# Kernel tuning notes

Hardware: AMD Instinct MI355X
Metric: run time of the kernel (lower is better)

Reference implementation:

```python
import jax, jax.numpy as jnp
import numpy as np

N_NODES = 50000
N_EDGES = 1_600_000
IN_DIM = 256
HIDDEN = 256
OUT_DIM = 48
K = 10
ALPHA = 0.5


def _ppr_temp(K, alpha):
    # PPR init from GPR_prop: temp[k] = alpha*(1-alpha)^k, temp[K] = (1-alpha)^K
    t = alpha * (1 - alpha) ** np.arange(K + 1, dtype=np.float32)
    t[-1] = (1 - alpha) ** K
    return jnp.asarray(t, dtype=jnp.float32)


def setup_inputs() -> dict:
    key = jax.random.key(0)
    ks = jax.random.split(key, 7)
    x = jax.random.normal(ks[0], (N_NODES, IN_DIM), dtype=jnp.float32)
    edge_index = jax.random.randint(ks[1], (2, N_EDGES), 0, N_NODES, dtype=jnp.int64)
    # Linear layers (torch Linear: y = x @ W.T + b); store as [in, out]
    lim1 = 1.0 / np.sqrt(IN_DIM)
    W1 = jax.random.uniform(ks[2], (IN_DIM, HIDDEN), jnp.float32, -lim1, lim1)
    b1 = jax.random.uniform(ks[3], (HIDDEN,), jnp.float32, -lim1, lim1)
    lim2 = 1.0 / np.sqrt(HIDDEN)
    W2 = jax.random.uniform(ks[4], (HIDDEN, OUT_DIM), jnp.float32, -lim2, lim2)
    b2 = jax.random.uniform(ks[5], (OUT_DIM,), jnp.float32, -lim2, lim2)
    temp = _ppr_temp(K, ALPHA)
    return {"x": x, "edge_index": edge_index, "W1": W1, "b1": b1,
            "W2": W2, "b2": b2, "temp": temp}


def reference(x, edge_index, W1, b1, W2, b2, temp):
    N = x.shape[0]
    # MLP head (dropout in eval mode -> identity)
    h = jax.nn.relu(x @ W1 + b1)
    h = h @ W2 + b2  # [N, OUT_DIM]

    # GCN normalization with self-loops: norm_e = deg^-1/2[src] * deg^-1/2[dst]
    loops = jnp.arange(N, dtype=edge_index.dtype)
    src = jnp.concatenate([edge_index[0], loops])
    dst = jnp.concatenate([edge_index[1], loops])
    deg = jnp.zeros((N,), dtype=h.dtype).at[dst].add(1.0)
    dinv = jax.lax.rsqrt(jnp.maximum(deg, 1e-12))
    norm = (dinv[src] * dinv[dst])[:, None]  # [E+N, 1]

    # K-hop propagation with learned gamma mixing
    def step(carry, gamma):
        hk, hidden = carry
        msg = norm * hk[src]                              # gather + scale
        hk = jax.ops.segment_sum(msg, dst, num_segments=N)  # scatter-add
        return (hk, hidden + gamma * hk), None

    (_, hidden), _ = jax.lax.scan(step, (h, temp[0] * h), temp[1:])
    return jax.nn.log_softmax(hidden, axis=1)
```

## Files before the change

### kernel.cpp

```cpp
#include <hip/hip_runtime.h>
#include <hip/hip_fp16.h>
#include <math.h>

#define BSH    9
#define BNODES 512
#define NBMAX  128
#define CAP2   24576
#define ECHUNK 6144

typedef short bf16x8 __attribute__((ext_vector_type(8)));
typedef float f32x4 __attribute__((ext_vector_type(4)));

__device__ __forceinline__ unsigned f2b(float f) {
    union { float f; unsigned u; } x; x.f = f;
    return (x.u + 0x7fffu + ((x.u >> 16) & 1u)) >> 16;
}


__global__ __launch_bounds__(256) void k_zero(int* __restrict__ p, int n) {
    int i = blockIdx.x * 256 + threadIdx.x;
    if (i < n) p[i] = 0;
}


__global__ __launch_bounds__(256) void k_castx(const float4* __restrict__ x, uint4* __restrict__ xb, int n8) {
    int i = blockIdx.x * 256 + threadIdx.x;
    if (i >= n8) return;
    float4 f0 = x[2 * i], f1 = x[2 * i + 1];
    uint4 o;
    o.x = f2b(f0.x) | (f2b(f0.y) << 16);
    o.y = f2b(f0.z) | (f2b(f0.w) << 16);
    o.z = f2b(f1.x) | (f2b(f1.y) << 16);
    o.w = f2b(f1.z) | (f2b(f1.w) << 16);
    xb[i] = o;
}

__global__ __launch_bounds__(256) void k_castw(const float* __restrict__ W1, const float* __restrict__ W2,
                                               unsigned short* __restrict__ w1t, unsigned short* __restrict__ w2t) {
    int i = blockIdx.x * 256 + threadIdx.x;
    if (i < 65536) {
        int n = i >> 8, k = i & 255;
        w1t[i] = (unsigned short)f2b(W1[k * 256 + n]);
    } else if (i < 65536 + 12288) {
        int j = i - 65536;
        int n = j >> 8, k = j & 255;
        w2t[j] = (unsigned short)f2b(W2[k * 48 + n]);
    }
}


__global__ __launch_bounds__(256) void k_bin(const int* __restrict__ src, const int* __restrict__ dst,
                                             int* __restrict__ bktcnt, unsigned* __restrict__ stage,
                                             int E, int NB) {
    __shared__ unsigned ecache[ECHUNK];
    __shared__ int lcnt[NBMAX], lbase[NBMAX], lcur[NBMAX];
    const int t = threadIdx.x;
    for (int i = t; i < NBMAX; i += 256) { lcnt[i] = 0; lcur[i] = 0; }
    const int e0 = blockIdx.x * ECHUNK;
    const int m = min(ECHUNK, E - e0);
    __syncthreads();
    for (int i = t; i < m; i += 256) {
        int s = src[e0 + i], d = dst[e0 + i];
        ecache[i] = ((unsigned)d << 16) | (unsigned)s;
        atomicAdd(&lcnt[d >> BSH], 1);
    }
    __syncthreads();
    if (t < NB) lbase[t] = lcnt[t] ? atomicAdd(&bktcnt[t], lcnt[t]) : 0;
    __syncthreads();
    for (int i = t; i < m; i += 256) {
        unsigned p = ecache[i];
        int b = (int)(p >> (16 + BSH));
        int pos = lbase[b] + atomicAdd(&lcur[b], 1);
        if (pos < CAP2) stage[(size_t)b * CAP2 + pos] = p;
    }
}


__global__ __launch_bounds__(512) void k_cnt(const unsigned* __restrict__ stage,
                                             const int* __restrict__ bktcnt,
                                             int* __restrict__ cnt,
                                             float* __restrict__ dinv, float* __restrict__ dinv2,
                                             float* __restrict__ sdeg, int N) {
    __shared__ int dcnt[BNODES];
    const int b = blockIdx.x, t = threadIdx.x;
    dcnt[t] = 0;
    __syncthreads();
    const int m = min(bktcnt[b], CAP2);
    const unsigned* st = stage + (size_t)b * CAP2;
    for (int i = t; i < m; i += 512)
        atomicAdd(&dcnt[(st[i] >> 16) & (BNODES - 1)], 1);
    __syncthreads();
    int node = b * BNODES + t;
    if (node <= N) {
        int c = dcnt[t];
        cnt[node] = c;
        float d = (float)c + 1.0f;
        float r = rsqrtf(d);
        dinv[node] = r;
        dinv2[node] = r * r;
        sdeg[node] = d * r;
    }
}


__global__ __launch_bounds__(256) void k_scan1(const int* __restrict__ cnt, int* __restrict__ rowptr,
                                               int* __restrict__ blk, int NT) {
    __shared__ int s[256];
    int t = threadIdx.x, i = blockIdx.x * 256 + t;
    int v = (i < NT) ? ((cnt[i] + 7) & ~7) : 0;
    s[t] = v; __syncthreads();
#pragma unroll
    for (int off = 1; off < 256; off <<= 1) {
        int x = (t >= off) ? s[t - off] : 0; __syncthreads();
        s[t] += x; __syncthreads();
    }
    if (i < NT) rowptr[i] = s[t] - v;
    if (t == 255) blk[blockIdx.x] = s[255];
}

__global__ __launch_bounds__(256) void k_scan2(int* __restrict__ blk, int nb) {
    __shared__ int s[256];
    int t = threadIdx.x;
    int v = (t < nb) ? blk[t] : 0;
    s[t] = v; __syncthreads();
#pragma unroll
    for (int off = 1; off < 256; off <<= 1) {
        int x = (t >= off) ? s[t - off] : 0; __syncthreads();
        s[t] += x; __syncthreads();
    }
    if (t < nb) blk[t] = s[t] - v;
}

__global__ __launch_bounds__(256) void k_scan3(int* __restrict__ rowptr, const int* __restrict__ blk, int NT) {
    int i = blockIdx.x * 256 + threadIdx.x;
    if (i < NT) rowptr[i] += blk[blockIdx.x];
}


__global__ __launch_bounds__(512) void k_place(const unsigned* __restrict__ stage,
                                               const int* __restrict__ bktcnt,
                                               const int* __restrict__ rowptr,
                                               unsigned short* __restrict__ csr, int N) {
    __shared__ int lcur[BNODES];
    const int b = blockIdx.x, t = threadIdx.x;
    const int node = b * BNODES + t;
    lcur[t] = (node < N) ? rowptr[node] : 0;
    __syncthreads();
    const int m = min(bktcnt[b], CAP2);
    const unsigned* st = stage + (size_t)b * CAP2;
    for (int i = t; i < m; i += 512) {
        unsigned p = st[i];
        int dl = (int)((p >> 16) & (BNODES - 1));
        int pos = atomicAdd(&lcur[dl], 1);
        csr[pos] = (unsigned short)(p & 0xffffu);
    }
    __syncthreads();
    if (node < N) {
        int e1 = rowptr[node + 1];
        for (int i = lcur[t]; i < e1; ++i) csr[i] = (unsigned short)N;
    }
}


__global__ __launch_bounds__(256) void k_mgemm1(const unsigned short* __restrict__ xb,
                                                const unsigned short* __restrict__ w1t,
                                                const float* __restrict__ bias,
                                                unsigned short* __restrict__ h1b, int M) {
    __shared__ unsigned short sbuf[128 * 136];
    unsigned short* As = sbuf;
    unsigned short* Bs = sbuf + 128 * 40;
    const int t = threadIdx.x;
    const int bm = blockIdx.x * 128;
    const int bn = blockIdx.y * 128;
    const int w = t >> 6, lane = t & 63;
    const int q = lane >> 4, l16 = lane & 15;

    f32x4 acc[2][8] = {};
    const int ar0 = t >> 2;
    const int kc  = t & 3;
    const int swz_st = ((kc ^ (ar0 & 3)) * 8);
    int gr0 = bm + ar0;       if (gr0 >= M) gr0 = M - 1;
    int gr1 = bm + ar0 + 64;  if (gr1 >= M) gr1 = M - 1;
    const int swz_rd = (q ^ (l16 & 3)) * 8;

    for (int k0 = 0; k0 < 256; k0 += 32) {
        uint4 a0 = *(const uint4*)&xb[(size_t)gr0 * 256 + k0 + kc * 8];
        uint4 a1 = *(const uint4*)&xb[(size_t)gr1 * 256 + k0 + kc * 8];
        uint4 b0 = *(const uint4*)&w1t[(size_t)(bn + ar0) * 256 + k0 + kc * 8];
        uint4 b1 = *(const uint4*)&w1t[(size_t)(bn + ar0 + 64) * 256 + k0 + kc * 8];
        __syncthreads();
        *(uint4*)&As[ar0 * 40 + swz_st] = a0;
        *(uint4*)&As[(ar0 + 64) * 40 + swz_st] = a1;
        *(uint4*)&Bs[ar0 * 40 + swz_st] = b0;
        *(uint4*)&Bs[(ar0 + 64) * 40 + swz_st] = b1;
        __syncthreads();
        bf16x8 af0 = *(bf16x8*)&As[(w * 32 + l16) * 40 + swz_rd];
        bf16x8 af1 = *(bf16x8*)&As[(w * 32 + 16 + l16) * 40 + swz_rd];
#pragma unroll
        for (int j = 0; j < 8; ++j) {
            bf16x8 bf = *(bf16x8*)&Bs[(j * 16 + l16) * 40 + swz_rd];
            acc[0][j] = __builtin_amdgcn_mfma_f32_16x16x32_bf16(af0, bf, acc[0][j], 0, 0, 0);
            acc[1][j] = __builtin_amdgcn_mfma_f32_16x16x32_bf16(af1, bf, acc[1][j], 0, 0, 0);
        }
    }
    __syncthreads();
#pragma unroll
    for (int j = 0; j < 8; ++j) {
        int col = j * 16 + l16;
        float bb = bias[bn + col];
#pragma unroll
        for (int i = 0; i < 2; ++i) {
#pragma unroll
            for (int r = 0; r < 4; ++r) {
                float v = fmaxf(acc[i][j][r] + bb, 0.f);
                sbuf[(w * 32 + i * 16 + q * 4 + r) * 136 + col] = (unsigned short)f2b(v);
            }
        }
    }
    __syncthreads();
    const int row = t >> 1;
    const int ch = (t & 1) * 64;
    if (bm + row < M) {
#pragma unroll
        for (int i = 0; i < 8; ++i) {
            uint4 v = *(uint4*)&sbuf[row * 136 + ch + i * 8];
            *(uint4*)&h1b[(size_t)(bm + row) * 256 + bn + ch + i * 8] = v;
        }
    }
}


__global__ __launch_bounds__(256) void k_mgemm2(const unsigned short* __restrict__ h1b,
                                                const unsigned short* __restrict__ w2t,
                                                const float* __restrict__ bias,
                                                const float* __restrict__ dinv,
                                                __half* __restrict__ u0, int M) {
    __shared__ unsigned short As[128 * 40];
    __shared__ unsigned short Bs[48 * 40];
    const int t = threadIdx.x;
    const int bm = blockIdx.x * 128;
    const int w = t >> 6, lane = t & 63;
    const int q = lane >> 4, l16 = lane & 15;

    f32x4 acc[2][3] = {};
    const int ar0 = t >> 2;
    const int kc  = t & 3;
    const int swz_st = ((kc ^ (ar0 & 3)) * 8);
    int gr0 = bm + ar0;      if (gr0 >= M) gr0 = M - 1;
    int gr1 = bm + ar0 + 64; if (gr1 >= M) gr1 = M - 1;
    const int swz_rd = (q ^ (l16 & 3)) * 8;

    for (int k0 = 0; k0 < 256; k0 += 32) {
        uint4 a0 = *(const uint4*)&h1b[(size_t)gr0 * 256 + k0 + kc * 8];
        uint4 a1 = *(const uint4*)&h1b[(size_t)gr1 * 256 + k0 + kc * 8];
        uint4 bv;
        if (t < 192) bv = *(const uint4*)&w2t[(size_t)ar0 * 256 + k0 + kc * 8];
        __syncthreads();
        *(uint4*)&As[ar0 * 40 + swz_st] = a0;
        *(uint4*)&As[(ar0 + 64) * 40 + swz_st] = a1;
        if (t < 192) *(uint4*)&Bs[ar0 * 40 + swz_st] = bv;
        __syncthreads();
        bf16x8 af0 = *(bf16x8*)&As[(w * 32 + l16) * 40 + swz_rd];
        bf16x8 af1 = *(bf16x8*)&As[(w * 32 + 16 + l16) * 40 + swz_rd];
#pragma unroll
        for (int j = 0; j < 3; ++j) {
            bf16x8 bf = *(bf16x8*)&Bs[(j * 16 + l16) * 40 + swz_rd];
            acc[0][j] = __builtin_amdgcn_mfma_f32_16x16x32_bf16(af0, bf, acc[0][j], 0, 0, 0);
            acc[1][j] = __builtin_amdgcn_mfma_f32_16x16x32_bf16(af1, bf, acc[1][j], 0, 0, 0);
        }
    }
#pragma unroll
    for (int j = 0; j < 3; ++j) {
        int col = j * 16 + l16;
        float bb = bias[col];
#pragma unroll
        for (int i = 0; i < 2; ++i) {
#pragma unroll
            for (int r = 0; r < 4; ++r) {
                int row = bm + w * 32 + i * 16 + q * 4 + r;
                if (row < M) {
                    float v = (acc[i][j][r] + bb) * dinv[row];
                    u0[(size_t)row * 64 + col] = __float2half(v);
                }
            }
        }
    }
}


__global__ __launch_bounds__(256) void k_hop(const __half* __restrict__ u, __half* __restrict__ unxt,
                                             const int* __restrict__ rowptr,
                                             const unsigned short* __restrict__ csr,
                                             const float* __restrict__ dinv2, int NT, int N) {
    int n = blockIdx.x * 4 + (threadIdx.x >> 6);
    if (n >= NT) return;
    const int lane = threadIdx.x & 63;
    const int c = lane & 7;
    const int j = lane >> 3;

    float acc[8] = {0.f, 0.f, 0.f, 0.f, 0.f, 0.f, 0.f, 0.f};
    const int e0 = rowptr[n], e1 = rowptr[n + 1];
    for (int e = e0; e < e1; e += 48) {
        const int rem = e1 - e;
        int t0 = (int)csr[e + j];
        int t1 = (int)csr[e + 8 + j];
        int t2 = (int)csr[e + 16 + j];
        int t3 = (int)csr[e + 24 + j];
        int t4 = (int)csr[e + 32 + j];
        int t5 = (int)csr[e + 40 + j];
        int s0 = t0;
        int s1 = (rem > 8)  ? t1 : N;
        int s2 = (rem > 16) ? t2 : N;
        int s3 = (rem > 24) ? t3 : N;
        int s4 = (rem > 32) ? t4 : N;
        int s5 = (rem > 40) ? t5 : N;
        union { uint4 u4; __half2 h2[4]; } g0, g1, g2, g3, g4, g5;
        g0.u4 = *(const uint4*)(u + (size_t)s0 * 64 + c * 8);
        g1.u4 = *(const uint4*)(u + (size_t)s1 * 64 + c * 8);
        g2.u4 = *(const uint4*)(u + (size_t)s2 * 64 + c * 8);
        g3.u4 = *(const uint4*)(u + (size_t)s3 * 64 + c * 8);
        g4.u4 = *(const uint4*)(u + (size_t)s4 * 64 + c * 8);
        g5.u4 = *(const uint4*)(u + (size_t)s5 * 64 + c * 8);
#pragma unroll
        for (int i = 0; i < 4; ++i) {
            float2 f0 = __half22float2(g0.h2[i]);
            float2 f1 = __half22float2(g1.h2[i]);
            float2 f2 = __half22float2(g2.h2[i]);
            float2 f3 = __half22float2(g3.h2[i]);
            float2 f4 = __half22float2(g4.h2[i]);
            float2 f5 = __half22float2(g5.h2[i]);
            acc[2 * i]     += ((f0.x + f1.x) + (f2.x + f3.x)) + (f4.x + f5.x);
            acc[2 * i + 1] += ((f0.y + f1.y) + (f2.y + f3.y)) + (f4.y + f5.y);
        }
    }
#pragma unroll
    for (int off = 8; off < 64; off <<= 1) {
#pragma unroll
        for (int i = 0; i < 8; ++i) acc[i] += __shfl_xor(acc[i], off);
    }
    if (j == 0 && c < 6) {
        union { uint4 u4; __half2 h2[4]; } sv, ov;
        sv.u4 = *(const uint4*)(u + (size_t)n * 64 + c * 8);
        float w2 = dinv2[n];
#pragma unroll
        for (int i = 0; i < 4; ++i) {
            float2 sf = __half22float2(sv.h2[i]);
            float2 r;
            r.x = (acc[2 * i]     + sf.x) * w2;
            r.y = (acc[2 * i + 1] + sf.y) * w2;
            ov.h2[i] = __float22half2_rn(r);
        }
        *(uint4*)(unxt + (size_t)n * 64 + c * 8) = ov.u4;
    }
}


__global__ __launch_bounds__(256) void k_final(const __half* __restrict__ u0, const __half* __restrict__ u1,
                                               size_t S, const float* __restrict__ sdeg,
                                               const float* __restrict__ temp,
                                               float* __restrict__ out, int N) {
    int w = (blockIdx.x * 256 + threadIdx.x) >> 6;
    int lane = threadIdx.x & 63;
    if (w >= N) return;
    size_t base = (size_t)w * 64 + lane;
    float val = 0.f, m = -INFINITY;
    if (lane < 48) {
        float acc = temp[0] * __half2float(u0[base]);
        const __half* uk = u1;
#pragma unroll
        for (int k = 1; k <= 10; ++k) {
            acc += temp[k] * __half2float(uk[base]);
            uk += S;
        }
        val = acc * sdeg[w];
        m = val;
    }
#pragma unroll
    for (int off = 32; off; off >>= 1) m = fmaxf(m, __shfl_xor(m, off));
    float ex = (lane < 48) ? __expf(val - m) : 0.f;
    float s = ex;
#pragma unroll
    for (int off = 32; off; off >>= 1) s += __shfl_xor(s, off);
    if (lane < 48) out[(size_t)w * 48 + lane] = val - m - __logf(s);
}


extern "C" void kernel_launch(void* const* d_in, const int* in_sizes, int n_in,
                              void* d_out, int out_size, void* d_ws, size_t ws_size,
                              hipStream_t stream) {
    const float* x    = (const float*)d_in[0];
    const int*   ei   = (const int*)d_in[1];
    const float* W1   = (const float*)d_in[2];
    const float* b1   = (const float*)d_in[3];
    const float* W2   = (const float*)d_in[4];
    const float* b2   = (const float*)d_in[5];
    const float* temp = (const float*)d_in[6];
    float* out = (float*)d_out;

    const int N = in_sizes[0] / 256;
    const int E = in_sizes[1] / 2;
    const int* src = ei;
    const int* dst = ei + E;

    const int NT  = N + 1;
    const int NT2 = N + 2;
    const int NB  = (NT + BNODES - 1) >> BSH;

    char* w8 = (char*)d_ws;
    size_t NP = (size_t)((NT2 + 63) & ~63);
    int*   cnt     = (int*)w8;
    int*   bktcnt  = cnt + NP;
    int*   rowptr  = bktcnt + 128;
    int*   blk     = rowptr + NP;
    float* dinv    = (float*)(blk + 256);
    float* dinv2   = dinv + NP;
    float* sdeg    = dinv2 + NP;
    unsigned short* csr = (unsigned short*)(sdeg + NP);
    size_t csr_i   = (((size_t)E + 32 * NT) / 2 + 32 + 63) & ~(size_t)63;
    unsigned short* w1t = (unsigned short*)((int*)(sdeg + NP) + csr_i);
    unsigned short* w2t = w1t + 65536;
    unsigned short* xb  = w2t + 12288 + 64;
    size_t S       = ((size_t)NT * 64 + 127) & ~(size_t)127;
    __half* u0     = (__half*)(xb + (size_t)N * 256);
    unsigned short* h1b = (unsigned short*)(u0 + S);
    unsigned* stage = (unsigned*)h1b;
    __half* u1     = (__half*)(h1b + (size_t)N * 256);

    const int nbS = (NT2 + 255) / 256;

    k_zero  <<<(int)((NP + 128 + 255) / 256), 256, 0, stream>>>(cnt, (int)(NP + 128));
    k_bin   <<<(E + ECHUNK - 1) / ECHUNK, 256, 0, stream>>>(src, dst, bktcnt, stage, E, NB);
    k_cnt   <<<NB, 512, 0, stream>>>(stage, bktcnt, cnt, dinv, dinv2, sdeg, N);
    k_scan1 <<<nbS, 256, 0, stream>>>(cnt, rowptr, blk, NT2);
    k_scan2 <<<1, 256, 0, stream>>>(blk, nbS);
    k_scan3 <<<nbS, 256, 0, stream>>>(rowptr, blk, NT2);
    k_place <<<NB, 512, 0, stream>>>(stage, bktcnt, rowptr, csr, N);

    k_castx <<<(N * 256 / 8 + 255) / 256, 256, 0, stream>>>((const float4*)x, (uint4*)xb, N * 256 / 8);
    k_castw <<<(65536 + 12288 + 255) / 256, 256, 0, stream>>>(W1, W2, w1t, w2t);

    dim3 g1((N + 127) / 128, 2);
    k_mgemm1<<<g1, 256, 0, stream>>>(xb, w1t, b1, h1b, N);
    k_mgemm2<<<(N + 127) / 128, 256, 0, stream>>>(h1b, w2t, b2, dinv, u0, N);
    k_zero  <<<1, 64, 0, stream>>>((int*)(u0 + (size_t)N * 64), 24);

    const int hopBlocks = (NT + 3) / 4;
    for (int k = 0; k < 10; ++k) {
        const __half* cur = (k == 0) ? u0 : (u1 + (size_t)(k - 1) * S);
        __half* nxt = u1 + (size_t)k * S;
        k_hop<<<hopBlocks, 256, 0, stream>>>(cur, nxt, rowptr, csr, dinv2, NT, N);
    }

    k_final<<<(N + 3) / 4, 256, 0, stream>>>(u0, u1, S, sdeg, temp, out, N);
}
```

Before: 463.9 us.

## Split each hop into two source-half passes to localize gathered features in cache

```diff
diff --git a/kernel.cpp b/kernel.cpp
--- a/kernel.cpp
+++ b/kernel.cpp
@@ -10,6 +10,7 @@
 
 typedef short bf16x8 __attribute__((ext_vector_type(8)));
 typedef float f32x4 __attribute__((ext_vector_type(4)));
+typedef unsigned u32x4 __attribute__((ext_vector_type(4)));
 
 __device__ __forceinline__ unsigned f2b(float f) {
     union { float f; unsigned u; } x; x.f = f;
@@ -78,22 +79,27 @@
 
 __global__ __launch_bounds__(512) void k_cnt(const unsigned* __restrict__ stage,
                                              const int* __restrict__ bktcnt,
-                                             int* __restrict__ cnt,
+                                             int* __restrict__ cnt, int* __restrict__ cntA,
                                              float* __restrict__ dinv, float* __restrict__ dinv2,
-                                             float* __restrict__ sdeg, int N) {
-    __shared__ int dcnt[BNODES];
+                                             float* __restrict__ sdeg, int N, int H) {
+    __shared__ int dcnt[BNODES], dcntA[BNODES];
     const int b = blockIdx.x, t = threadIdx.x;
-    dcnt[t] = 0;
+    dcnt[t] = 0; dcntA[t] = 0;
     __syncthreads();
     const int m = min(bktcnt[b], CAP2);
     const unsigned* st = stage + (size_t)b * CAP2;
-    for (int i = t; i < m; i += 512)
-        atomicAdd(&dcnt[(st[i] >> 16) & (BNODES - 1)], 1);
+    for (int i = t; i < m; i += 512) {
+        unsigned p = st[i];
+        int dl = (int)((p >> 16) & (BNODES - 1));
+        atomicAdd(&dcnt[dl], 1);
+        if ((int)(p & 0xffffu) < H) atomicAdd(&dcntA[dl], 1);
+    }
     __syncthreads();
     int node = b * BNODES + t;
     if (node <= N) {
         int c = dcnt[t];
         cnt[node] = c;
+        cntA[node] = dcntA[t];
         float d = (float)c + 1.0f;
         float r = rsqrtf(d);
         dinv[node] = r;
@@ -103,11 +109,15 @@
 }
 
 
-__global__ __launch_bounds__(256) void k_scan1(const int* __restrict__ cnt, int* __restrict__ rowptr,
-                                               int* __restrict__ blk, int NT) {
+__global__ __launch_bounds__(256) void k_scan1(const int* __restrict__ cnt, const int* __restrict__ cntA,
+                                               int* __restrict__ rowptr, int* __restrict__ blk, int NT) {
     __shared__ int s[256];
     int t = threadIdx.x, i = blockIdx.x * 256 + t;
-    int v = (i < NT) ? ((cnt[i] + 7) & ~7) : 0;
+    int v = 0;
+    if (i < NT) {
+        int c = cnt[i], cA = cntA[i];
+        v = ((cA + 7) & ~7) + ((c - cA + 7) & ~7);
+    }
     s[t] = v; __syncthreads();
 #pragma unroll
     for (int off = 1; off < 256; off <<= 1) {
@@ -131,33 +141,44 @@
     if (t < nb) blk[t] = s[t] - v;
 }
 
-__global__ __launch_bounds__(256) void k_scan3(int* __restrict__ rowptr, const int* __restrict__ blk, int NT) {
+__global__ __launch_bounds__(256) void k_scan3(int* __restrict__ rowptr, int* __restrict__ rowmid,
+                                               const int* __restrict__ cntA,
+                                               const int* __restrict__ blk, int NT2, int NT) {
     int i = blockIdx.x * 256 + threadIdx.x;
-    if (i < NT) rowptr[i] += blk[blockIdx.x];
+    if (i < NT2) {
+        int r = rowptr[i] + blk[blockIdx.x];
+        rowptr[i] = r;
+        if (i < NT) rowmid[i] = r + ((cntA[i] + 7) & ~7);
+    }
 }
 
 
 __global__ __launch_bounds__(512) void k_place(const unsigned* __restrict__ stage,
                                                const int* __restrict__ bktcnt,
                                                const int* __restrict__ rowptr,
-                                               unsigned short* __restrict__ csr, int N) {
-    __shared__ int lcur[BNODES];
+                                               const int* __restrict__ rowmid,
+                                               unsigned short* __restrict__ csr, int N, int H) {
+    __shared__ int lcurA[BNODES], lcurB[BNODES];
     const int b = blockIdx.x, t = threadIdx.x;
     const int node = b * BNODES + t;
-    lcur[t] = (node < N) ? rowptr[node] : 0;
+    lcurA[t] = (node < N) ? rowptr[node] : 0;
+    lcurB[t] = (node < N) ? rowmid[node] : 0;
     __syncthreads();
     const int m = min(bktcnt[b], CAP2);
     const unsigned* st = stage + (size_t)b * CAP2;
     for (int i = t; i < m; i += 512) {
         unsigned p = st[i];
         int dl = (int)((p >> 16) & (BNODES - 1));
-        int pos = atomicAdd(&lcur[dl], 1);
-        csr[pos] = (unsigned short)(p & 0xffffu);
+        int s = (int)(p & 0xffffu);
+        int pos = (s < H) ? atomicAdd(&lcurA[dl], 1) : atomicAdd(&lcurB[dl], 1);
+        csr[pos] = (unsigned short)s;
     }
     __syncthreads();
     if (node < N) {
+        int midv = rowmid[node];
+        for (int i = lcurA[t]; i < midv; ++i) csr[i] = (unsigned short)N;
         int e1 = rowptr[node + 1];
-        for (int i = lcur[t]; i < e1; ++i) csr[i] = (unsigned short)N;
+        for (int i = lcurB[t]; i < e1; ++i) csr[i] = (unsigned short)N;
     }
 }
 
@@ -289,9 +310,9 @@
 
 
 __global__ __launch_bounds__(256) void k_hop(const __half* __restrict__ u, __half* __restrict__ unxt,
-                                             const int* __restrict__ rowptr,
+                                             const int* __restrict__ starts, const int* __restrict__ ends,
                                              const unsigned short* __restrict__ csr,
-                                             const float* __restrict__ dinv2, int NT, int N) {
+                                             const float* __restrict__ dinv2, int NT, int N, int fin) {
     int n = blockIdx.x * 4 + (threadIdx.x >> 6);
     if (n >= NT) return;
     const int lane = threadIdx.x & 63;
@@ -299,38 +320,30 @@
     const int j = lane >> 3;
 
     float acc[8] = {0.f, 0.f, 0.f, 0.f, 0.f, 0.f, 0.f, 0.f};
-    const int e0 = rowptr[n], e1 = rowptr[n + 1];
-    for (int e = e0; e < e1; e += 48) {
+    const int e0 = starts[n], e1 = ends[n];
+    for (int e = e0; e < e1; e += 32) {
         const int rem = e1 - e;
         int t0 = (int)csr[e + j];
         int t1 = (int)csr[e + 8 + j];
         int t2 = (int)csr[e + 16 + j];
         int t3 = (int)csr[e + 24 + j];
-        int t4 = (int)csr[e + 32 + j];
-        int t5 = (int)csr[e + 40 + j];
         int s0 = t0;
         int s1 = (rem > 8)  ? t1 : N;
         int s2 = (rem > 16) ? t2 : N;
         int s3 = (rem > 24) ? t3 : N;
-        int s4 = (rem > 32) ? t4 : N;
-        int s5 = (rem > 40) ? t5 : N;
-        union { uint4 u4; __half2 h2[4]; } g0, g1, g2, g3, g4, g5;
+        union { uint4 u4; __half2 h2[4]; } g0, g1, g2, g3;
         g0.u4 = *(const uint4*)(u + (size_t)s0 * 64 + c * 8);
         g1.u4 = *(const uint4*)(u + (size_t)s1 * 64 + c * 8);
         g2.u4 = *(const uint4*)(u + (size_t)s2 * 64 + c * 8);
         g3.u4 = *(const uint4*)(u + (size_t)s3 * 64 + c * 8);
-        g4.u4 = *(const uint4*)(u + (size_t)s4 * 64 + c * 8);
-        g5.u4 = *(const uint4*)(u + (size_t)s5 * 64 + c * 8);
 #pragma unroll
         for (int i = 0; i < 4; ++i) {
-            float2 f0 = __half22float2(g0.h2[i]);
-            float2 f1 = __half22float2(g1.h2[i]);
-            float2 f2 = __half22float2(g2.h2[i]);
-            float2 f3 = __half22float2(g3.h2[i]);
-            float2 f4 = __half22float2(g4.h2[i]);
-            float2 f5 = __half22float2(g5.h2[i]);
-            acc[2 * i]     += ((f0.x + f1.x) + (f2.x + f3.x)) + (f4.x + f5.x);
-            acc[2 * i + 1] += ((f0.y + f1.y) + (f2.y + f3.y)) + (f4.y + f5.y);
+            __half2 p  = __hadd2(g0.h2[i], g1.h2[i]);
+            __half2 qq = __hadd2(g2.h2[i], g3.h2[i]);
+            float2 fp = __half22float2(p);
+            float2 fq = __half22float2(qq);
+            acc[2 * i]     += fp.x + fq.x;
+            acc[2 * i + 1] += fp.y + fq.y;
         }
     }
 #pragma unroll
@@ -339,18 +352,31 @@
         for (int i = 0; i < 8; ++i) acc[i] += __shfl_xor(acc[i], off);
     }
     if (j == 0 && c < 6) {
-        union { uint4 u4; __half2 h2[4]; } sv, ov;
-        sv.u4 = *(const uint4*)(u + (size_t)n * 64 + c * 8);
-        float w2 = dinv2[n];
-#pragma unroll
-        for (int i = 0; i < 4; ++i) {
-            float2 sf = __half22float2(sv.h2[i]);
-            float2 r;
-            r.x = (acc[2 * i]     + sf.x) * w2;
-            r.y = (acc[2 * i + 1] + sf.y) * w2;
-            ov.h2[i] = __float22half2_rn(r);
-        }
-        *(uint4*)(unxt + (size_t)n * 64 + c * 8) = ov.u4;
+        union { u32x4 v; __half2 h2[4]; } ov;
+        if (fin) {
+            union { uint4 u4; __half2 h2[4]; } sv, pv;
+            sv.u4 = *(const uint4*)(u + (size_t)n * 64 + c * 8);
+            pv.u4 = *(const uint4*)(unxt + (size_t)n * 64 + c * 8);
+            float w2 = dinv2[n];
+#pragma unroll
+            for (int i = 0; i < 4; ++i) {
+                float2 sf = __half22float2(sv.h2[i]);
+                float2 pf = __half22float2(pv.h2[i]);
+                float2 r;
+                r.x = (acc[2 * i]     + pf.x + sf.x) * w2;
+                r.y = (acc[2 * i + 1] + pf.y + sf.y) * w2;
+                ov.h2[i] = __float22half2_rn(r);
+            }
+        } else {
+#pragma unroll
+            for (int i = 0; i < 4; ++i) {
+                float2 r;
+                r.x = acc[2 * i];
+                r.y = acc[2 * i + 1];
+                ov.h2[i] = __float22half2_rn(r);
+            }
+        }
+        __builtin_nontemporal_store(ov.v, (u32x4*)(unxt + (size_t)n * 64 + c * 8));
     }
 }
 
@@ -405,13 +431,16 @@
     const int NT  = N + 1;
     const int NT2 = N + 2;
     const int NB  = (NT + BNODES - 1) >> BSH;
+    const int H   = N / 2;
 
     char* w8 = (char*)d_ws;
     size_t NP = (size_t)((NT2 + 63) & ~63);
     int*   cnt     = (int*)w8;
-    int*   bktcnt  = cnt + NP;
+    int*   cntA    = cnt + NP;
+    int*   bktcnt  = cntA + NP;
     int*   rowptr  = bktcnt + 128;
-    int*   blk     = rowptr + NP;
+    int*   rowmid  = rowptr + NP;
+    int*   blk     = rowmid + NP;
     float* dinv    = (float*)(blk + 256);
     float* dinv2   = dinv + NP;
     float* sdeg    = dinv2 + NP;
@@ -428,13 +457,13 @@
 
     const int nbS = (NT2 + 255) / 256;
 
-    k_zero  <<<(int)((NP + 128 + 255) / 256), 256, 0, stream>>>(cnt, (int)(NP + 128));
+    k_zero  <<<(int)((2 * NP + 128 + 255) / 256), 256, 0, stream>>>(cnt, (int)(2 * NP + 128));
     k_bin   <<<(E + ECHUNK - 1) / ECHUNK, 256, 0, stream>>>(src, dst, bktcnt, stage, E, NB);
-    k_cnt   <<<NB, 512, 0, stream>>>(stage, bktcnt, cnt, dinv, dinv2, sdeg, N);
-    k_scan1 <<<nbS, 256, 0, stream>>>(cnt, rowptr, blk, NT2);
+    k_cnt   <<<NB, 512, 0, stream>>>(stage, bktcnt, cnt, cntA, dinv, dinv2, sdeg, N, H);
+    k_scan1 <<<nbS, 256, 0, stream>>>(cnt, cntA, rowptr, blk, NT2);
     k_scan2 <<<1, 256, 0, stream>>>(blk, nbS);
-    k_scan3 <<<nbS, 256, 0, stream>>>(rowptr, blk, NT2);
-    k_place <<<NB, 512, 0, stream>>>(stage, bktcnt, rowptr, csr, N);
+    k_scan3 <<<nbS, 256, 0, stream>>>(rowptr, rowmid, cntA, blk, NT2, NT);
+    k_place <<<NB, 512, 0, stream>>>(stage, bktcnt, rowptr, rowmid, csr, N, H);
 
     k_castx <<<(N * 256 / 8 + 255) / 256, 256, 0, stream>>>((const float4*)x, (uint4*)xb, N * 256 / 8);
     k_castw <<<(65536 + 12288 + 255) / 256, 256, 0, stream>>>(W1, W2, w1t, w2t);
@@ -448,7 +477,8 @@
     for (int k = 0; k < 10; ++k) {
         const __half* cur = (k == 0) ? u0 : (u1 + (size_t)(k - 1) * S);
         __half* nxt = u1 + (size_t)k * S;
-        k_hop<<<hopBlocks, 256, 0, stream>>>(cur, nxt, rowptr, csr, dinv2, NT, N);
+        k_hop<<<hopBlocks, 256, 0, stream>>>(cur, nxt, rowptr, rowmid, csr, dinv2, NT, N, 0);
+        k_hop<<<hopBlocks, 256, 0, stream>>>(cur, nxt, rowmid, rowptr + 1, csr, dinv2, NT, N, 1);
     }
 
     k_final<<<(N + 3) / 4, 256, 0, stream>>>(u0, u1, S, sdeg, temp, out, N);
```

New measurement: 614.1 us. 32.4% more time.
